# Optimization experiments

Measured on AMD Instinct MI355X. Metric: run time of the kernel, lower is better.

The kernel has to match this reference:

```python
import jax, jax.numpy as jnp
import numpy as np
from jax import lax

PLANES = 384
N_POINTS = 4
KERNEL_SIZE = 11
INIT_RADIUS = 2.0 * (2.0 / KERNEL_SIZE)


def setup_inputs() -> dict:
    key = jax.random.key(0)
    k1, k2, k3 = jax.random.split(key, 3)
    x = jax.random.normal(k1, (16, PLANES, 64, 64), dtype=jnp.float32)
    # trunc_normal_(std=0.2, a=-1, b=1) approximated by clipped normal
    weight_coord = jnp.clip(0.2 * jax.random.normal(k2, (1, N_POINTS, 2), dtype=jnp.float32), -1.0, 1.0)
    radius = jnp.full((1, N_POINTS, 1, 1), INIT_RADIUS, dtype=jnp.float32)
    weights = 0.02 * jax.random.normal(k3, (1, PLANES, N_POINTS), dtype=jnp.float32)
    return {"x": x, "weight_coord": weight_coord, "radius": radius, "weights": weights}


def _make_kernels(weight_coord, radius, weights):
    K = KERNEL_SIZE
    lin = jnp.linspace(-1.0, 1.0, K)
    # torch.meshgrid default 'ij' indexing, stacked on dim 0 -> (2, K, K)
    gy, gx = jnp.meshgrid(lin, lin, indexing="ij")
    kernel_coord = jnp.stack([gy, gx], axis=0).reshape(2, K * K)  # (2, K*K)
    # diff: (1, n_points, K*K, 2)
    diff = weight_coord[:, :, None, :] - kernel_coord.T[None, None, :, :]
    diff = jnp.transpose(diff, (0, 1, 3, 2)).reshape(1, N_POINTS, 2, K, K)
    # L1 hat function per point: (1, n_points, K, K)
    d = jax.nn.relu(1.0 - jnp.abs(diff).sum(axis=2) / radius)
    # mix points into per-channel kernels: (1, planes, K*K) -> (planes, K, K)
    kernels = jnp.matmul(weights, d.reshape(1, N_POINTS, K * K)).reshape(PLANES, K, K)
    # torch: flip(permute(0,2,1), dims=(1,))
    kernels = jnp.flip(jnp.transpose(kernels, (0, 2, 1)), axis=1)
    return kernels


def reference(x, weight_coord, radius, weights):
    kernels = _make_kernels(weight_coord, radius, weights)  # (planes, K, K)
    pad = KERNEL_SIZE // 2
    out = lax.conv_general_dilated(
        x,
        kernels[:, None, :, :],  # (O=planes, I/g=1, K, K)
        window_strides=(1, 1),
        padding=[(pad, pad), (pad, pad)],
        dimension_numbers=("NCHW", "OIHW", "NCHW"),
        feature_group_count=PLANES,
    )
    return out
```

## Files before the change

### kernel.cpp

```cpp
#include <hip/hip_runtime.h>

#define PLANES 384
#define K 11
#define TS 96
#define ROWS 74

__global__ __launch_bounds__(256) void smpconv_kernel(
    const float* __restrict__ x,
    const float* __restrict__ wcoord,
    const float* __restrict__ radius,
    const float* __restrict__ wts,
    float* __restrict__ out)
{
    __shared__ __align__(16) float tile[ROWS * TS];
    __shared__ __align__(16) float skv[12 * 12];
    __shared__ int s_rowmask, s_colmask;

    const int tid = threadIdx.x;
    const int bid = blockIdx.x;
    const int c   = bid % PLANES;

    #pragma unroll
    for (int z = 0; z < 7; ++z) {
        int e = z * 256 + tid;
        if (e < (ROWS * TS) / 4) {
            float4 zz; zz.x = zz.y = zz.z = zz.w = 0.f;
            *(float4*)&tile[e * 4] = zz;
        }
    }
    if (tid == 0) { s_rowmask = 0; s_colmask = 0; }
    __syncthreads();

    const float* xp = x + (size_t)bid * 4096;
    #pragma unroll
    for (int it = 0; it < 4; ++it) {
        int e = it * 256 + tid;
        float4 v = ((const float4*)xp)[e];
        int gy = e >> 4;
        int gx = (e & 15) << 2;
        *(float4*)&tile[(gy + 5) * TS + gx + 8] = v;
    }
    if (tid < K * K) {
        int i = tid / K;
        int j = tid - i * K;
        float la = -1.f + 0.2f * (float)j;
        float lb = -1.f + 0.2f * (float)(10 - i);
        float a = 0.f;
        #pragma unroll
        for (int p = 0; p < 4; ++p) {
            float ir = 1.f / radius[p];
            float t = 1.f - (fabsf(wcoord[2*p] - la) + fabsf(wcoord[2*p+1] - lb)) * ir;
            t = fmaxf(t, 0.f);
            a = fmaf(wts[c*4 + p], t, a);
        }
        skv[i * 12 + j] = a;
        if (a != 0.f) {
            atomicOr(&s_rowmask, 1 << i);
            atomicOr(&s_colmask, 1 << j);
        }
    }
    __syncthreads();

    const int rowmask = __builtin_amdgcn_readfirstlane(s_rowmask);
    const int colmask = __builtin_amdgcn_readfirstlane(s_colmask);

    const int ty = tid >> 4;
    const int tx = tid & 15;

    float acc[4][4];
    #pragma unroll
    for (int o = 0; o < 4; ++o)
        #pragma unroll
        for (int xx = 0; xx < 4; ++xx) acc[o][xx] = 0.f;

    float kvs[4][12];
    #pragma unroll
    for (int s = 0; s < 4; ++s)
        #pragma unroll
        for (int j = 0; j < 12; ++j) kvs[s][j] = 0.f;

    const float* rowbase = &tile[(ty * 4) * TS + tx * 4];

    #pragma unroll
    for (int rr = 0; rr < 14; ++rr) {
        if (rr < K) {
            if ((rowmask >> rr) & 1) {
                float4 k0 = *(const float4*)&skv[rr*12 + 0];
                float4 k1 = *(const float4*)&skv[rr*12 + 4];
                float4 k2 = *(const float4*)&skv[rr*12 + 8];
                const int s = rr & 3;
                kvs[s][0]=k0.x; kvs[s][1]=k0.y; kvs[s][2]=k0.z; kvs[s][3]=k0.w;
                kvs[s][4]=k1.x; kvs[s][5]=k1.y; kvs[s][6]=k1.z; kvs[s][7]=k1.w;
                kvs[s][8]=k2.x; kvs[s][9]=k2.y; kvs[s][10]=k2.z; kvs[s][11]=k2.w;
            }
        }
        const int need = ((rowmask << 3) >> rr) & 0xF;
        if (need) {
            const float* rp = rowbase + rr * TS;
            float4 q0 = *(const float4*)(rp + 0);
            float4 q1 = *(const float4*)(rp + 4);
            float4 q2 = *(const float4*)(rp + 8);
            float4 q3 = *(const float4*)(rp + 12);
            float4 q4 = *(const float4*)(rp + 16);
            float w[20];
            w[0]=q0.x;  w[1]=q0.y;  w[2]=q0.z;  w[3]=q0.w;
            w[4]=q1.x;  w[5]=q1.y;  w[6]=q1.z;  w[7]=q1.w;
            w[8]=q2.x;  w[9]=q2.y;  w[10]=q2.z; w[11]=q2.w;
            w[12]=q3.x; w[13]=q3.y; w[14]=q3.z; w[15]=q3.w;
            w[16]=q4.x; w[17]=q4.y; w[18]=q4.z; w[19]=q4.w;
            #pragma unroll
            for (int o = 0; o < 4; ++o) {
                if ((need >> (3 - o)) & 1) {
                    const int s = (rr - o) & 3;
                    #pragma unroll
                    for (int j = 0; j < K; ++j) {
                        if ((colmask >> j) & 1) {
                            const float kv = kvs[s][j];
                            #pragma unroll
                            for (int xx = 0; xx < 4; ++xx)
                                acc[o][xx] = fmaf(w[xx + j + 3], kv, acc[o][xx]);
                        }
                    }
                }
            }
        }
    }

    float* op = out + (size_t)bid * 4096 + (ty * 4) * 64 + tx * 4;
    #pragma unroll
    for (int o = 0; o < 4; ++o) {
        float4 v;
        v.x = acc[o][0]; v.y = acc[o][1]; v.z = acc[o][2]; v.w = acc[o][3];
        *(float4*)(op + o * 64) = v;
    }
}

extern "C" void kernel_launch(void* const* d_in, const int* in_sizes, int n_in,
                              void* d_out, int out_size, void* d_ws, size_t ws_size,
                              hipStream_t stream) {
    const float* x      = (const float*)d_in[0];
    const float* wcoord = (const float*)d_in[1];
    const float* radius = (const float*)d_in[2];
    const float* wts    = (const float*)d_in[3];
    float* out          = (float*)d_out;

    const int nplanes = 16 * PLANES;
    smpconv_kernel<<<dim3(nplanes), dim3(256), 0, stream>>>(x, wcoord, radius, wts, out);
}
```

Measured before the change: 209.5 us.

## Use per-row column masks to skip zero taps and pad LDS rows

Replaces the single row/column sparsity masks with a per-kernel-row column mask, so each row's FMAs skip only that row's zero taps instead of the union of all columns. Skips shared-memory loads of kernel vectors and input float4 chunks that no nonzero tap needs. Adds a row-dependent padding offset to the LDS tile layout, likely to reduce bank conflicts. This brings more uniform-branch overhead and more registers for the per-row masks.

```diff
diff --git a/kernel.cpp b/kernel.cpp
--- a/kernel.cpp
+++ b/kernel.cpp
@@ -14,7 +14,7 @@
 {
     __shared__ __align__(16) float tile[ROWS * TS];
     __shared__ __align__(16) float skv[12 * 12];
-    __shared__ int s_rowmask, s_colmask;
+    __shared__ int s_rcmask[K];
 
     const int tid = threadIdx.x;
     const int bid = blockIdx.x;
@@ -28,7 +28,7 @@
             *(float4*)&tile[e * 4] = zz;
         }
     }
-    if (tid == 0) { s_rowmask = 0; s_colmask = 0; }
+    if (tid < K) s_rcmask[tid] = 0;
     __syncthreads();
 
     const float* xp = x + (size_t)bid * 4096;
@@ -38,7 +38,8 @@
         float4 v = ((const float4*)xp)[e];
         int gy = e >> 4;
         int gx = (e & 15) << 2;
-        *(float4*)&tile[(gy + 5) * TS + gx + 8] = v;
+        int row = gy + 5;
+        *(float4*)&tile[row * TS + (row & 12) + gx + 8] = v;
     }
     if (tid < K * K) {
         int i = tid / K;
@@ -54,71 +55,76 @@
             a = fmaf(wts[c*4 + p], t, a);
         }
         skv[i * 12 + j] = a;
-        if (a != 0.f) {
-            atomicOr(&s_rowmask, 1 << i);
-            atomicOr(&s_colmask, 1 << j);
-        }
+        if (a != 0.f) atomicOr(&s_rcmask[i], 1 << j);
     }
     __syncthreads();
 
-    const int rowmask = __builtin_amdgcn_readfirstlane(s_rowmask);
-    const int colmask = __builtin_amdgcn_readfirstlane(s_colmask);
+    int rc[K];
+    int rowmask = 0, colmask = 0;
+    #pragma unroll
+    for (int i = 0; i < K; ++i) {
+        rc[i] = __builtin_amdgcn_readfirstlane(s_rcmask[i]);
+        if (rc[i]) rowmask |= 1 << i;
+        colmask |= rc[i];
+    }
+    const bool nq0 = (colmask & 0x001) != 0;
+    const bool nq1 = (colmask & 0x01F) != 0;
+    const bool nq2 = (colmask & 0x1FC) != 0;
+    const bool nq3 = (colmask & 0x7C0) != 0;
+    const bool nq4 = (colmask & 0x400) != 0;
 
     const int ty = tid >> 4;
     const int tx = tid & 15;
 
-    float acc[4][4];
-    #pragma unroll
-    for (int o = 0; o < 4; ++o)
-        #pragma unroll
-        for (int xx = 0; xx < 4; ++xx) acc[o][xx] = 0.f;
+    float acc[4][4] = {};
+    float kvs[4][12] = {};
 
-    float kvs[4][12];
-    #pragma unroll
-    for (int s = 0; s < 4; ++s)
-        #pragma unroll
-        for (int j = 0; j < 12; ++j) kvs[s][j] = 0.f;
-
-    const float* rowbase = &tile[(ty * 4) * TS + tx * 4];
+    const float* colbase = tile + tx * 4;
 
     #pragma unroll
     for (int rr = 0; rr < 14; ++rr) {
         if (rr < K) {
             if ((rowmask >> rr) & 1) {
-                float4 k0 = *(const float4*)&skv[rr*12 + 0];
-                float4 k1 = *(const float4*)&skv[rr*12 + 4];
-                float4 k2 = *(const float4*)&skv[rr*12 + 8];
                 const int s = rr & 3;
-                kvs[s][0]=k0.x; kvs[s][1]=k0.y; kvs[s][2]=k0.z; kvs[s][3]=k0.w;
-                kvs[s][4]=k1.x; kvs[s][5]=k1.y; kvs[s][6]=k1.z; kvs[s][7]=k1.w;
-                kvs[s][8]=k2.x; kvs[s][9]=k2.y; kvs[s][10]=k2.z; kvs[s][11]=k2.w;
+                const int m = rc[rr];
+                if (m & 0x00F) {
+                    float4 k = *(const float4*)&skv[rr*12 + 0];
+                    kvs[s][0]=k.x; kvs[s][1]=k.y; kvs[s][2]=k.z; kvs[s][3]=k.w;
+                }
+                if (m & 0x0F0) {
+                    float4 k = *(const float4*)&skv[rr*12 + 4];
+                    kvs[s][4]=k.x; kvs[s][5]=k.y; kvs[s][6]=k.z; kvs[s][7]=k.w;
+                }
+                if (m & 0x700) {
+                    float4 k = *(const float4*)&skv[rr*12 + 8];
+                    kvs[s][8]=k.x; kvs[s][9]=k.y; kvs[s][10]=k.z;
+                }
             }
         }
         const int need = ((rowmask << 3) >> rr) & 0xF;
         if (need) {
-            const float* rp = rowbase + rr * TS;
-            float4 q0 = *(const float4*)(rp + 0);
-            float4 q1 = *(const float4*)(rp + 4);
-            float4 q2 = *(const float4*)(rp + 8);
-            float4 q3 = *(const float4*)(rp + 12);
-            float4 q4 = *(const float4*)(rp + 16);
+            const int row = ty * 4 + rr;
+            const float* rp = colbase + row * TS + (row & 12);
             float w[20];
-            w[0]=q0.x;  w[1]=q0.y;  w[2]=q0.z;  w[3]=q0.w;
-            w[4]=q1.x;  w[5]=q1.y;  w[6]=q1.z;  w[7]=q1.w;
-            w[8]=q2.x;  w[9]=q2.y;  w[10]=q2.z; w[11]=q2.w;
-            w[12]=q3.x; w[13]=q3.y; w[14]=q3.z; w[15]=q3.w;
-            w[16]=q4.x; w[17]=q4.y; w[18]=q4.z; w[19]=q4.w;
+            if (nq0) { float4 v = *(const float4*)(rp + 0);  w[0]=v.x;  w[1]=v.y;  w[2]=v.z;  w[3]=v.w; }
+            if (nq1) { float4 v = *(const float4*)(rp + 4);  w[4]=v.x;  w[5]=v.y;  w[6]=v.z;  w[7]=v.w; }
+            if (nq2) { float4 v = *(const float4*)(rp + 8);  w[8]=v.x;  w[9]=v.y;  w[10]=v.z; w[11]=v.w; }
+            if (nq3) { float4 v = *(const float4*)(rp + 12); w[12]=v.x; w[13]=v.y; w[14]=v.z; w[15]=v.w; }
+            if (nq4) { float4 v = *(const float4*)(rp + 16); w[16]=v.x; w[17]=v.y; w[18]=v.z; w[19]=v.w; }
             #pragma unroll
             for (int o = 0; o < 4; ++o) {
-                if ((need >> (3 - o)) & 1) {
-                    const int s = (rr - o) & 3;
-                    #pragma unroll
-                    for (int j = 0; j < K; ++j) {
-                        if ((colmask >> j) & 1) {
-                            const float kv = kvs[s][j];
-                            #pragma unroll
-                            for (int xx = 0; xx < 4; ++xx)
-                                acc[o][xx] = fmaf(w[xx + j + 3], kv, acc[o][xx]);
+                if (rr - o >= 0 && rr - o < K) {
+                    if ((need >> (3 - o)) & 1) {
+                        const int m = rc[rr - o];
+                        const int s = (rr - o) & 3;
+                        #pragma unroll
+                        for (int j = 0; j < K; ++j) {
+                            if ((m >> j) & 1) {
+                                const float kv = kvs[s][j];
+                                #pragma unroll
+                                for (int xx = 0; xx < 4; ++xx)
+                                    acc[o][xx] = fmaf(w[xx + j + 3], kv, acc[o][xx]);
+                            }
                         }
                     }
                 }
```

New measurement: 255.7 us. 22.0% more time.

## Split each plane into two half-height blocks with smaller padded LDS tile

Applied to the files above, without the earlier changes.

Each block now handles 32 output rows of one plane instead of 64, doubling the grid. Each thread computes 2 rows by 4 columns instead of 4 by 4. The shared tile shrinks to 42 rows with stride 92 plus a per-row offset to spread LDS banks. The aim is lower LDS use and register pressure, so more blocks fit per CU with better latency hiding. The cost is halo rows loaded twice, kernel weights computed per half-block, and less register reuse of each loaded row.

```diff
diff --git a/kernel.cpp b/kernel.cpp
--- a/kernel.cpp
+++ b/kernel.cpp
@@ -2,8 +2,8 @@
 
 #define PLANES 384
 #define K 11
-#define TS 96
-#define ROWS 74
+#define TS 92
+#define LROWS 42
 
 __global__ __launch_bounds__(256) void smpconv_kernel(
     const float* __restrict__ x,
@@ -12,18 +12,20 @@
     const float* __restrict__ wts,
     float* __restrict__ out)
 {
-    __shared__ __align__(16) float tile[ROWS * TS];
+    __shared__ __align__(16) float tile[LROWS * TS];
     __shared__ __align__(16) float skv[12 * 12];
     __shared__ int s_rowmask, s_colmask;
 
-    const int tid = threadIdx.x;
-    const int bid = blockIdx.x;
-    const int c   = bid % PLANES;
+    const int tid   = threadIdx.x;
+    const int bid   = blockIdx.x;
+    const int plane = bid >> 1;
+    const int base  = (bid & 1) << 5;
+    const int c     = plane % PLANES;
 
     #pragma unroll
-    for (int z = 0; z < 7; ++z) {
+    for (int z = 0; z < 4; ++z) {
         int e = z * 256 + tid;
-        if (e < (ROWS * TS) / 4) {
+        if (e < (LROWS * TS) / 4) {
             float4 zz; zz.x = zz.y = zz.z = zz.w = 0.f;
             *(float4*)&tile[e * 4] = zz;
         }
@@ -31,14 +33,19 @@
     if (tid == 0) { s_rowmask = 0; s_colmask = 0; }
     __syncthreads();
 
-    const float* xp = x + (size_t)bid * 4096;
+    const float4* xp4 = (const float4*)(x + (size_t)plane * 4096);
     #pragma unroll
-    for (int it = 0; it < 4; ++it) {
+    for (int it = 0; it < 3; ++it) {
         int e = it * 256 + tid;
-        float4 v = ((const float4*)xp)[e];
-        int gy = e >> 4;
-        int gx = (e & 15) << 2;
-        *(float4*)&tile[(gy + 5) * TS + gx + 8] = v;
+        if (e < LROWS * 16) {
+            int r   = e >> 4;
+            int gx4 = e & 15;
+            int prow = base - 5 + r;
+            if (prow >= 0 && prow < 64) {
+                float4 v = xp4[prow * 16 + gx4];
+                *(float4*)&tile[r * TS + (r & 12) + 8 + (gx4 << 2)] = v;
+            }
+        }
     }
     if (tid < K * K) {
         int i = tid / K;
@@ -67,36 +74,30 @@
     const int ty = tid >> 4;
     const int tx = tid & 15;
 
-    float acc[4][4];
+    float acc0[4] = {0.f, 0.f, 0.f, 0.f};
+    float acc1[4] = {0.f, 0.f, 0.f, 0.f};
+    float kvs[2][12];
     #pragma unroll
-    for (int o = 0; o < 4; ++o)
-        #pragma unroll
-        for (int xx = 0; xx < 4; ++xx) acc[o][xx] = 0.f;
-
-    float kvs[4][12];
-    #pragma unroll
-    for (int s = 0; s < 4; ++s)
+    for (int s = 0; s < 2; ++s)
         #pragma unroll
         for (int j = 0; j < 12; ++j) kvs[s][j] = 0.f;
 
-    const float* rowbase = &tile[(ty * 4) * TS + tx * 4];
-
     #pragma unroll
-    for (int rr = 0; rr < 14; ++rr) {
-        if (rr < K) {
-            if ((rowmask >> rr) & 1) {
-                float4 k0 = *(const float4*)&skv[rr*12 + 0];
-                float4 k1 = *(const float4*)&skv[rr*12 + 4];
-                float4 k2 = *(const float4*)&skv[rr*12 + 8];
-                const int s = rr & 3;
-                kvs[s][0]=k0.x; kvs[s][1]=k0.y; kvs[s][2]=k0.z; kvs[s][3]=k0.w;
-                kvs[s][4]=k1.x; kvs[s][5]=k1.y; kvs[s][6]=k1.z; kvs[s][7]=k1.w;
-                kvs[s][8]=k2.x; kvs[s][9]=k2.y; kvs[s][10]=k2.z; kvs[s][11]=k2.w;
-            }
+    for (int rr = 0; rr < 12; ++rr) {
+        const bool n0 = (rr < K)  && ((rowmask >> rr) & 1);
+        const bool n1 = (rr >= 1) && ((rowmask >> (rr - 1)) & 1);
+        if (n0) {
+            const int s = rr & 1;
+            float4 k0 = *(const float4*)&skv[rr*12 + 0];
+            float4 k1 = *(const float4*)&skv[rr*12 + 4];
+            float4 k2 = *(const float4*)&skv[rr*12 + 8];
+            kvs[s][0]=k0.x; kvs[s][1]=k0.y; kvs[s][2]=k0.z; kvs[s][3]=k0.w;
+            kvs[s][4]=k1.x; kvs[s][5]=k1.y; kvs[s][6]=k1.z; kvs[s][7]=k1.w;
+            kvs[s][8]=k2.x; kvs[s][9]=k2.y; kvs[s][10]=k2.z; kvs[s][11]=k2.w;
         }
-        const int need = ((rowmask << 3) >> rr) & 0xF;
-        if (need) {
-            const float* rp = rowbase + rr * TS;
+        if (n0 || n1) {
+            const int row = 2 * ty + rr;
+            const float* rp = &tile[row * TS + (row & 12) + tx * 4];
             float4 q0 = *(const float4*)(rp + 0);
             float4 q1 = *(const float4*)(rp + 4);
             float4 q2 = *(const float4*)(rp + 8);
@@ -108,31 +109,38 @@
             w[8]=q2.x;  w[9]=q2.y;  w[10]=q2.z; w[11]=q2.w;
             w[12]=q3.x; w[13]=q3.y; w[14]=q3.z; w[15]=q3.w;
             w[16]=q4.x; w[17]=q4.y; w[18]=q4.z; w[19]=q4.w;
-            #pragma unroll
-            for (int o = 0; o < 4; ++o) {
-                if ((need >> (3 - o)) & 1) {
-                    const int s = (rr - o) & 3;
-                    #pragma unroll
-                    for (int j = 0; j < K; ++j) {
-                        if ((colmask >> j) & 1) {
-                            const float kv = kvs[s][j];
-                            #pragma unroll
-                            for (int xx = 0; xx < 4; ++xx)
-                                acc[o][xx] = fmaf(w[xx + j + 3], kv, acc[o][xx]);
-                        }
+            if (n0) {
+                const int s = rr & 1;
+                #pragma unroll
+                for (int j = 0; j < K; ++j) {
+                    if ((colmask >> j) & 1) {
+                        const float kv = kvs[s][j];
+                        #pragma unroll
+                        for (int xx = 0; xx < 4; ++xx)
+                            acc0[xx] = fmaf(w[xx + j + 3], kv, acc0[xx]);
+                    }
+                }
+            }
+            if (n1) {
+                const int s = (rr - 1) & 1;
+                #pragma unroll
+                for (int j = 0; j < K; ++j) {
+                    if ((colmask >> j) & 1) {
+                        const float kv = kvs[s][j];
+                        #pragma unroll
+                        for (int xx = 0; xx < 4; ++xx)
+                            acc1[xx] = fmaf(w[xx + j + 3], kv, acc1[xx]);
                     }
                 }
             }
         }
     }
 
-    float* op = out + (size_t)bid * 4096 + (ty * 4) * 64 + tx * 4;
-    #pragma unroll
-    for (int o = 0; o < 4; ++o) {
-        float4 v;
-        v.x = acc[o][0]; v.y = acc[o][1]; v.z = acc[o][2]; v.w = acc[o][3];
-        *(float4*)(op + o * 64) = v;
-    }
+    float* op = out + (size_t)plane * 4096 + (base + 2 * ty) * 64 + tx * 4;
+    float4 v0; v0.x = acc0[0]; v0.y = acc0[1]; v0.z = acc0[2]; v0.w = acc0[3];
+    float4 v1; v1.x = acc1[0]; v1.y = acc1[1]; v1.z = acc1[2]; v1.w = acc1[3];
+    *(float4*)(op)      = v0;
+    *(float4*)(op + 64) = v1;
 }
 
 extern "C" void kernel_launch(void* const* d_in, const int* in_sizes, int n_in,
@@ -144,6 +152,6 @@
     const float* wts    = (const float*)d_in[3];
     float* out          = (float*)d_out;
 
-    const int nplanes = 16 * PLANES;
-    smpconv_kernel<<<dim3(nplanes), dim3(256), 0, stream>>>(x, wcoord, radius, wts, out);
+    const int nblocks = 16 * PLANES * 2;
+    smpconv_kernel<<<dim3(nblocks), dim3(256), 0, stream>>>(x, wcoord, radius, wts, out);
 }
```

Result: slower. 228.0 us (+8.8%).

## Use per-row column masks to skip zero taps and re-pad LDS tile

Applied to the files above, without the earlier changes.

Replaces the global row/column nonzero masks with a per-row column mask, so each kernel row only issues FMAs for its own nonzero taps instead of the union of all columns. The shared-memory tile stride drops from 96 to 88 with a row-dependent offset, to change bank mapping and reduce LDS bank conflicts. This costs extra scalar registers for the 11 row masks plus more uniform branching, and slightly more complex address arithmetic.

```diff
diff --git a/kernel.cpp b/kernel.cpp
--- a/kernel.cpp
+++ b/kernel.cpp
@@ -2,7 +2,7 @@
 
 #define PLANES 384
 #define K 11
-#define TS 96
+#define TS 88
 #define ROWS 74
 
 __global__ __launch_bounds__(256) void smpconv_kernel(
@@ -12,9 +12,9 @@
     const float* __restrict__ wts,
     float* __restrict__ out)
 {
-    __shared__ __align__(16) float tile[ROWS * TS];
+    __shared__ __align__(16) float tile[ROWS * TS + 16];
     __shared__ __align__(16) float skv[12 * 12];
-    __shared__ int s_rowmask, s_colmask;
+    __shared__ int s_rcmask[K];
 
     const int tid = threadIdx.x;
     const int bid = blockIdx.x;
@@ -23,12 +23,12 @@
     #pragma unroll
     for (int z = 0; z < 7; ++z) {
         int e = z * 256 + tid;
-        if (e < (ROWS * TS) / 4) {
+        if (e < (ROWS * TS + 16) / 4) {
             float4 zz; zz.x = zz.y = zz.z = zz.w = 0.f;
             *(float4*)&tile[e * 4] = zz;
         }
     }
-    if (tid == 0) { s_rowmask = 0; s_colmask = 0; }
+    if (tid < K) s_rcmask[tid] = 0;
     __syncthreads();
 
     const float* xp = x + (size_t)bid * 4096;
@@ -38,7 +38,8 @@
         float4 v = ((const float4*)xp)[e];
         int gy = e >> 4;
         int gx = (e & 15) << 2;
-        *(float4*)&tile[(gy + 5) * TS + gx + 8] = v;
+        int row = gy + 5;
+        *(float4*)&tile[row * TS + (row & 12) + 8 + gx] = v;
     }
     if (tid < K * K) {
         int i = tid / K;
@@ -54,41 +55,34 @@
             a = fmaf(wts[c*4 + p], t, a);
         }
         skv[i * 12 + j] = a;
-        if (a != 0.f) {
-            atomicOr(&s_rowmask, 1 << i);
-            atomicOr(&s_colmask, 1 << j);
-        }
+        if (a != 0.f) atomicOr(&s_rcmask[i], 1 << j);
     }
     __syncthreads();
 
-    const int rowmask = __builtin_amdgcn_readfirstlane(s_rowmask);
-    const int colmask = __builtin_amdgcn_readfirstlane(s_colmask);
+    int rc[K];
+    int rowmask = 0;
+    #pragma unroll
+    for (int i = 0; i < K; ++i) {
+        rc[i] = __builtin_amdgcn_readfirstlane(s_rcmask[i]);
+        if (rc[i]) rowmask |= 1 << i;
+    }
 
     const int ty = tid >> 4;
     const int tx = tid & 15;
 
-    float acc[4][4];
-    #pragma unroll
-    for (int o = 0; o < 4; ++o)
-        #pragma unroll
-        for (int xx = 0; xx < 4; ++xx) acc[o][xx] = 0.f;
+    float acc[4][4] = {};
+    float kvs[4][12] = {};
 
-    float kvs[4][12];
-    #pragma unroll
-    for (int s = 0; s < 4; ++s)
-        #pragma unroll
-        for (int j = 0; j < 12; ++j) kvs[s][j] = 0.f;
-
-    const float* rowbase = &tile[(ty * 4) * TS + tx * 4];
+    const float* colbase = tile + tx * 4;
 
     #pragma unroll
     for (int rr = 0; rr < 14; ++rr) {
         if (rr < K) {
             if ((rowmask >> rr) & 1) {
+                const int s = rr & 3;
                 float4 k0 = *(const float4*)&skv[rr*12 + 0];
                 float4 k1 = *(const float4*)&skv[rr*12 + 4];
                 float4 k2 = *(const float4*)&skv[rr*12 + 8];
-                const int s = rr & 3;
                 kvs[s][0]=k0.x; kvs[s][1]=k0.y; kvs[s][2]=k0.z; kvs[s][3]=k0.w;
                 kvs[s][4]=k1.x; kvs[s][5]=k1.y; kvs[s][6]=k1.z; kvs[s][7]=k1.w;
                 kvs[s][8]=k2.x; kvs[s][9]=k2.y; kvs[s][10]=k2.z; kvs[s][11]=k2.w;
@@ -96,7 +90,8 @@
         }
         const int need = ((rowmask << 3) >> rr) & 0xF;
         if (need) {
-            const float* rp = rowbase + rr * TS;
+            const int row = ty * 4 + rr;
+            const float* rp = colbase + row * TS + (row & 12);
             float4 q0 = *(const float4*)(rp + 0);
             float4 q1 = *(const float4*)(rp + 4);
             float4 q2 = *(const float4*)(rp + 8);
@@ -110,15 +105,18 @@
             w[16]=q4.x; w[17]=q4.y; w[18]=q4.z; w[19]=q4.w;
             #pragma unroll
             for (int o = 0; o < 4; ++o) {
-                if ((need >> (3 - o)) & 1) {
-                    const int s = (rr - o) & 3;
-                    #pragma unroll
-                    for (int j = 0; j < K; ++j) {
-                        if ((colmask >> j) & 1) {
-                            const float kv = kvs[s][j];
-                            #pragma unroll
-                            for (int xx = 0; xx < 4; ++xx)
-                                acc[o][xx] = fmaf(w[xx + j + 3], kv, acc[o][xx]);
+                if (rr - o >= 0 && rr - o < K) {
+                    if ((need >> (3 - o)) & 1) {
+                        const int m = rc[rr - o];
+                        const int s = (rr - o) & 3;
+                        #pragma unroll
+                        for (int j = 0; j < K; ++j) {
+                            if ((m >> j) & 1) {
+                                const float kv = kvs[s][j];
+                                #pragma unroll
+                                for (int xx = 0; xx < 4; ++xx)
+                                    acc[o][xx] = fmaf(w[xx + j + 3], kv, acc[o][xx]);
+                            }
                         }
                     }
                 }
```

New measurement: 209.1 us. Within noise of the previous version (-0.2%).
